# Optimization experiments

Hardware: AMD Instinct MI355X
Metric: run time of the kernel (lower is better)

Reference implementation:

```python
import jax, jax.numpy as jnp
import numpy as np


def setup_inputs() -> dict:
    key = jax.random.key(0)
    k1, k2 = jax.random.split(key)
    N, C, H, W = 16, 256, 128, 128
    CLS = 9
    feat = jax.random.normal(k1, (N, C, H, W), dtype=jnp.float32)
    logit = jax.random.normal(k2, (N, CLS, H, W), dtype=jnp.float32)
    return {"feat": feat, "logit": logit, "cls_num": CLS}


def reference(feat, logit, cls_num):
    # gen_prototypes from MVNet.
    # NOTE: the torch code indexes feat[label == c] where feat is [n, h*w, C]
    # and label is [n, h*w]; the 2-D boolean mask flattens the batch dim, so
    # every sample's "prototypes" are the SAME global per-class mean over all
    # batch pixels. We reproduce that exactly with one segment reduction.
    n, c, h, w = feat.shape
    p = n * h * w  # total pixels across batch
    feat_f = feat.transpose(0, 2, 3, 1).reshape(p, c)            # [P, C]
    label = jnp.argmax(logit.transpose(0, 2, 3, 1).reshape(p, -1), axis=-1)  # [P]
    sums = jax.ops.segment_sum(feat_f, label, num_segments=cls_num)          # [cls, C]
    counts = jax.ops.segment_sum(jnp.ones((p,), feat.dtype), label,
                                 num_segments=cls_num)                       # [cls]
    # empty class -> sum over empty set = 0 (torch's sum(0) branch);
    # nonempty -> mean. Dividing by max(count,1) gives both cases.
    protos = sums / jnp.maximum(counts, jnp.asarray(1.0, feat.dtype))[:, None]
    protos = protos.T  # [C, cls] (torch permutes (1,0))
    return jnp.broadcast_to(protos[None], (n, c, cls_num))  # [n, C, cls]
```

## Files before the change

kernel.cpp:

```cpp
#include <hip/hip_runtime.h>

#define HWN   16384
#define NB    16
#define CH    256
#define CLS   9
#define PTOT  (NB * HWN)
#define LBLK  (PTOT / 1024)
#define SBLK  (NB * CH)

typedef float v4f __attribute__((ext_vector_type(4)));

__global__ __launch_bounds__(256) void label_kernel(
    const float* __restrict__ logit,
    unsigned int* __restrict__ labels4,
    int* __restrict__ hist)
{
    __shared__ int h[CLS];
    if (threadIdx.x < CLS) h[threadIdx.x] = 0;
    __syncthreads();

    const int t  = blockIdx.x * 256 + threadIdx.x;
    const int p0 = t << 2;
    const int n  = p0 >> 14;
    const int hw = p0 & (HWN - 1);
    const v4f* base = (const v4f*)(logit + (size_t)n * CLS * HWN + hw);

    v4f best = __builtin_nontemporal_load(base);
    int b0 = 0, b1 = 0, b2 = 0, b3 = 0;
#pragma unroll
    for (int k = 1; k < CLS; ++k) {
        const v4f v = __builtin_nontemporal_load(base + (size_t)k * (HWN / 4));
        if (v[0] > best[0]) { best[0] = v[0]; b0 = k; }
        if (v[1] > best[1]) { best[1] = v[1]; b1 = k; }
        if (v[2] > best[2]) { best[2] = v[2]; b2 = k; }
        if (v[3] > best[3]) { best[3] = v[3]; b3 = k; }
    }
    labels4[t] = (unsigned)b0 | ((unsigned)b1 << 8) |
                 ((unsigned)b2 << 16) | ((unsigned)b3 << 24);

    atomicAdd(&h[b0], 1); atomicAdd(&h[b1], 1);
    atomicAdd(&h[b2], 1); atomicAdd(&h[b3], 1);
    __syncthreads();
    if (threadIdx.x < CLS) hist[blockIdx.x * CLS + threadIdx.x] = h[threadIdx.x];
}

__global__ __launch_bounds__(256) void sum_kernel(
    const float* __restrict__ feat,
    const unsigned int* __restrict__ labels4,
    float* __restrict__ partial)
{
    const int b = blockIdx.x;
    const int n = b >> 8;

    const v4f*          f4 = (const v4f*)(feat + (size_t)b * HWN);
    const unsigned int* l4 = labels4 + (size_t)n * (HWN / 4);

    float s[CLS];
#pragma unroll
    for (int k = 0; k < CLS; ++k) s[k] = 0.0f;

#pragma unroll 8
    for (int i = threadIdx.x; i < HWN / 4; i += 256) {
        const v4f          v  = __builtin_nontemporal_load(&f4[i]);
        const unsigned int lu = l4[i];
#pragma unroll
        for (int j = 0; j < 4; ++j) {
            const float x = v[j];
            const int   l = (lu >> (8 * j)) & 255;
#pragma unroll
            for (int k = 0; k < CLS; ++k)
                s[k] += (l == k) ? x : 0.0f;
        }
    }

#pragma unroll
    for (int k = 0; k < CLS; ++k)
        for (int off = 32; off > 0; off >>= 1)
            s[k] += __shfl_down(s[k], off, 64);

    __shared__ float wsum[4][CLS];
    const int wave = threadIdx.x >> 6;
    if ((threadIdx.x & 63) == 0) {
#pragma unroll
        for (int k = 0; k < CLS; ++k) wsum[wave][k] = s[k];
    }
    __syncthreads();

    if (threadIdx.x < CLS) {
        const int k = threadIdx.x;
        partial[b * CLS + k] = wsum[0][k] + wsum[1][k] + wsum[2][k] + wsum[3][k];
    }
}

__global__ __launch_bounds__(256) void finalize_kernel(
    const float* __restrict__ partial,
    const int* __restrict__ hist,
    float* __restrict__ out)
{
    __shared__ int sc[256][CLS];
    const int t = threadIdx.x;
#pragma unroll
    for (int k = 0; k < CLS; ++k) sc[t][k] = hist[t * CLS + k];
    __syncthreads();
#pragma unroll
    for (int off = 128; off > 0; off >>= 1) {
        if (t < off) {
#pragma unroll
            for (int k = 0; k < CLS; ++k) sc[t][k] += sc[t + off][k];
        }
        __syncthreads();
    }

    const int idx = blockIdx.x * 256 + t;
    if (idx >= CH * CLS) return;
    const int k = idx % CLS;

    float acc = 0.0f;
#pragma unroll
    for (int np = 0; np < NB; ++np)
        acc += partial[np * (CH * CLS) + idx];

    const float proto = acc / (float)max(sc[0][k], 1);
#pragma unroll
    for (int np = 0; np < NB; ++np)
        out[np * (CH * CLS) + idx] = proto;
}

extern "C" void kernel_launch(void* const* d_in, const int* in_sizes, int n_in,
                              void* d_out, int out_size, void* d_ws, size_t ws_size,
                              hipStream_t stream)
{
    const float* feat  = (const float*)d_in[0];
    const float* logit = (const float*)d_in[1];

    char* ws = (char*)d_ws;
    float*        partial = (float*)ws;
    int*          hist    = (int*)(ws + 147456);
    unsigned int* labels4 = (unsigned int*)(ws + 156928);

    label_kernel<<<LBLK, 256, 0, stream>>>(logit, labels4, hist);
    sum_kernel<<<SBLK, 256, 0, stream>>>(feat, labels4, partial);
    finalize_kernel<<<(CH * CLS + 255) / 256, 256, 0, stream>>>(partial, hist, (float*)d_out);
}
```

Before: 353.0 us.

## Process four channels per block in sum kernel with mask-FMA accumulation

The sum kernel now has each block handle four channels of one sample, so every label word it loads is reused across four feature rows. The per-pixel class compare-select becomes a 0/1 mask multiplied into FMA accumulators. The mask is built once and shared across the four channels, and the final reduction moves from wave shuffles to a shared-memory transpose. Nontemporal loads are also replaced with plain loads in both kernels. The cost is higher register pressure (36 accumulators plus 36 mask values), a large shared-memory reduction buffer, and only a quarter as many blocks.

```diff
diff --git a/kernel.cpp b/kernel.cpp
--- a/kernel.cpp
+++ b/kernel.cpp
@@ -7,6 +7,8 @@
 #define PTOT  (NB * HWN)
 #define LBLK  (PTOT / 1024)
 #define SBLK  (NB * CH)
+#define CGRP  (CH / 4)
+#define SUMB  (NB * CGRP)
 
 typedef float v4f __attribute__((ext_vector_type(4)));
 
@@ -23,13 +25,13 @@
     const int p0 = t << 2;
     const int n  = p0 >> 14;
     const int hw = p0 & (HWN - 1);
-    const v4f* base = (const v4f*)(logit + (size_t)n * CLS * HWN + hw);
+    const v4f* __restrict__ base = (const v4f*)(logit + (size_t)n * CLS * HWN + hw);
 
-    v4f best = __builtin_nontemporal_load(base);
+    v4f best = base[0];
     int b0 = 0, b1 = 0, b2 = 0, b3 = 0;
 #pragma unroll
     for (int k = 1; k < CLS; ++k) {
-        const v4f v = __builtin_nontemporal_load(base + (size_t)k * (HWN / 4));
+        const v4f v = base[(size_t)k * (HWN / 4)];
         if (v[0] > best[0]) { best[0] = v[0]; b0 = k; }
         if (v[1] > best[1]) { best[1] = v[1]; b1 = k; }
         if (v[2] > best[2]) { best[2] = v[2]; b2 = k; }
@@ -49,46 +51,75 @@
     const unsigned int* __restrict__ labels4,
     float* __restrict__ partial)
 {
-    const int b = blockIdx.x;
-    const int n = b >> 8;
+    const int b  = blockIdx.x;
+    const int n  = b >> 6;
+    const int cg = b & (CGRP - 1);
+    const int c0 = (n << 8) + (cg << 2);
 
-    const v4f*          f4 = (const v4f*)(feat + (size_t)b * HWN);
-    const unsigned int* l4 = labels4 + (size_t)n * (HWN / 4);
+    const v4f* __restrict__ f0 = (const v4f*)(feat + (size_t)(c0 + 0) * HWN);
+    const v4f* __restrict__ f1 = (const v4f*)(feat + (size_t)(c0 + 1) * HWN);
+    const v4f* __restrict__ f2 = (const v4f*)(feat + (size_t)(c0 + 2) * HWN);
+    const v4f* __restrict__ f3 = (const v4f*)(feat + (size_t)(c0 + 3) * HWN);
+    const unsigned int* __restrict__ l4 = labels4 + (size_t)n * (HWN / 4);
 
-    float s[CLS];
+    float acc[4][CLS];
 #pragma unroll
-    for (int k = 0; k < CLS; ++k) s[k] = 0.0f;
+    for (int c = 0; c < 4; ++c)
+#pragma unroll
+        for (int k = 0; k < CLS; ++k) acc[c][k] = 0.0f;
 
-#pragma unroll 8
+#pragma unroll 2
     for (int i = threadIdx.x; i < HWN / 4; i += 256) {
-        const v4f          v  = __builtin_nontemporal_load(&f4[i]);
         const unsigned int lu = l4[i];
+        const v4f x0 = f0[i];
+        const v4f x1 = f1[i];
+        const v4f x2 = f2[i];
+        const v4f x3 = f3[i];
+
+        float m[4][CLS];
 #pragma unroll
         for (int j = 0; j < 4; ++j) {
-            const float x = v[j];
-            const int   l = (lu >> (8 * j)) & 255;
+            const int l = (lu >> (8 * j)) & 255;
 #pragma unroll
-            for (int k = 0; k < CLS; ++k)
-                s[k] += (l == k) ? x : 0.0f;
+            for (int k = 0; k < CLS; ++k) {
+                float mm = (l == k) ? 1.0f : 0.0f;
+                asm("" : "+v"(mm));
+                m[j][k] = mm;
+            }
+        }
+
+#pragma unroll
+        for (int k = 0; k < CLS; ++k) {
+            acc[0][k] += x0[0] * m[0][k] + x0[1] * m[1][k]
+                       + x0[2] * m[2][k] + x0[3] * m[3][k];
+            acc[1][k] += x1[0] * m[0][k] + x1[1] * m[1][k]
+                       + x1[2] * m[2][k] + x1[3] * m[3][k];
+            acc[2][k] += x2[0] * m[0][k] + x2[1] * m[1][k]
+                       + x2[2] * m[2][k] + x2[3] * m[3][k];
+            acc[3][k] += x3[0] * m[0][k] + x3[1] * m[1][k]
+                       + x3[2] * m[2][k] + x3[3] * m[3][k];
         }
     }
 
+    __shared__ float red[256][37];
 #pragma unroll
-    for (int k = 0; k < CLS; ++k)
-        for (int off = 32; off > 0; off >>= 1)
-            s[k] += __shfl_down(s[k], off, 64);
-
-    __shared__ float wsum[4][CLS];
-    const int wave = threadIdx.x >> 6;
-    if ((threadIdx.x & 63) == 0) {
+    for (int c = 0; c < 4; ++c)
 #pragma unroll
-        for (int k = 0; k < CLS; ++k) wsum[wave][k] = s[k];
-    }
+        for (int k = 0; k < CLS; ++k) red[threadIdx.x][c * CLS + k] = acc[c][k];
     __syncthreads();
 
-    if (threadIdx.x < CLS) {
-        const int k = threadIdx.x;
-        partial[b * CLS + k] = wsum[0][k] + wsum[1][k] + wsum[2][k] + wsum[3][k];
+    if (threadIdx.x < 36) {
+        float s0 = 0.0f, s1 = 0.0f, s2 = 0.0f, s3 = 0.0f;
+#pragma unroll 8
+        for (int t = 0; t < 256; t += 4) {
+            s0 += red[t + 0][threadIdx.x];
+            s1 += red[t + 1][threadIdx.x];
+            s2 += red[t + 2][threadIdx.x];
+            s3 += red[t + 3][threadIdx.x];
+        }
+        const int c = threadIdx.x / CLS;
+        const int k = threadIdx.x - c * CLS;
+        partial[(size_t)(c0 + c) * CLS + k] = (s0 + s1) + (s2 + s3);
     }
 }
 
@@ -139,6 +170,6 @@
     unsigned int* labels4 = (unsigned int*)(ws + 156928);
 
     label_kernel<<<LBLK, 256, 0, stream>>>(logit, labels4, hist);
-    sum_kernel<<<SBLK, 256, 0, stream>>>(feat, labels4, partial);
+    sum_kernel<<<SUMB, 256, 0, stream>>>(feat, labels4, partial);
     finalize_kernel<<<(CH * CLS + 255) / 256, 256, 0, stream>>>(partial, hist, (float*)d_out);
 }
```

Result: slower. 373.2 us (+5.7%).
